# Kernel optimization log

Measured on AMD Instinct MI355X. Metric: run time of the kernel, lower is better.

The kernel has to match this reference:

```python
import jax, jax.numpy as jnp
import numpy as np

N = 50000
E = 800000
F0, F1, F2 = 256, 128, 64
EPS = 1e-5


def setup_inputs() -> dict:
    key = jax.random.key(0)
    ks = jax.random.split(key, 20)
    x = jax.random.normal(ks[0], (N, F0), dtype=jnp.float32)
    src = jax.random.randint(ks[1], (E,), 0, N)
    dst = jax.random.randint(ks[2], (E,), 0, N)
    edge_index = jnp.stack([src, dst]).astype(jnp.int64)

    def lin(k, fi, fo):
        s = 1.0 / np.sqrt(fi)
        k1, k2 = jax.random.split(k)
        W = jax.random.uniform(k1, (fi, fo), minval=-s, maxval=s, dtype=jnp.float32)
        b = jax.random.uniform(k2, (fo,), minval=-s, maxval=s, dtype=jnp.float32)
        return W, b

    We1, be1 = lin(ks[3], F0, F1)
    We2, be2 = lin(ks[4], F1, F2)
    Wd1, bd1 = lin(ks[5], F2, F1)
    Wd2, bd2 = lin(ks[6], F1, F0)
    return {
        'x': x, 'edge_index': edge_index,
        'We1': We1, 'be1': be1, 'g1': jnp.ones((F1,)), 'bb1': jnp.zeros((F1,)),
        'We2': We2, 'be2': be2, 'g2': jnp.ones((F2,)), 'bb2': jnp.zeros((F2,)),
        'Wd1': Wd1, 'bd1': bd1, 'g3': jnp.ones((F1,)), 'bb3': jnp.zeros((F1,)),
        'Wd2': Wd2, 'bd2': bd2, 'g4': jnp.ones((F0,)), 'bb4': jnp.zeros((F0,)),
    }


def _gcn(x, W, b, src, dst, dinv_src_dst, dinv_self):
    # PyG GCNConv: linear first, then sym-normalized propagation with self-loops
    h = x @ W + b                               # [N, Fout]
    msg = h[src] * dinv_src_dst[:, None]        # [E, Fout]
    out = jax.ops.segment_sum(msg, dst, num_segments=N)
    return out + h * dinv_self[:, None]         # self-loop term


def _bn(x, g, b):
    # BatchNorm1d training-mode: biased batch stats over node dim
    m = jnp.mean(x, axis=0)
    v = jnp.mean(jnp.square(x - m), axis=0)
    return g * (x - m) * jax.lax.rsqrt(v + EPS) + b


def reference(x, edge_index, We1, be1, g1, bb1, We2, be2, g2, bb2,
              Wd1, bd1, g3, bb3, Wd2, bd2, g4, bb4):
    src, dst = edge_index[0], edge_index[1]
    deg = jnp.zeros((N,), x.dtype).at[dst].add(1.0) + 1.0  # in-degree + self-loop
    dinv = jax.lax.rsqrt(deg)
    dsd = dinv[src] * dinv[dst]
    dself = dinv * dinv

    relu = jax.nn.relu
    # Encoder block 0 (outer i==0): relu(GCN), relu(BN)
    h = relu(_gcn(x, We1, be1, src, dst, dsd, dself))
    h = relu(_bn(h, g1, bb1))
    enc1 = h
    # Encoder block 1 (outer i==1 == len(inner)-1): relu(GCN), BN (no relu)
    h = relu(_gcn(h, We2, be2, src, dst, dsd, dself))
    h = _bn(h, g2, bb2)
    enc2 = h
    # Decoder block 0: relu(GCN), relu(BN)
    h = relu(_gcn(h, Wd1, bd1, src, dst, dsd, dself))
    h = relu(_bn(h, g3, bb3))
    # Decoder block 1 (i==1): relu(GCN), BN (no relu)
    h = relu(_gcn(h, Wd2, bd2, src, dst, dsd, dself))
    h = _bn(h, g4, bb4)
    # AE returns (reconstruction, encoded_embeddings)
    return h, enc1, enc2
```

## Files before the change

### kernel.cpp

```cpp
#include <hip/hip_runtime.h>

#define N_NODES 50000
#define F0 256
#define F1 128
#define F2 64
#define BN_EPS 1e-5f

typedef float f32x4 __attribute__((ext_vector_type(4)));
typedef __bf16 bf16x8 __attribute__((ext_vector_type(8)));
typedef unsigned short ushort8v __attribute__((ext_vector_type(8)));

__device__ __forceinline__ float bflo(unsigned v) { return __uint_as_float(v << 16); }
__device__ __forceinline__ float bfhi(unsigned v) { return __uint_as_float(v & 0xFFFF0000u); }
__device__ __forceinline__ unsigned short f2bf(float f) {
  unsigned u = __float_as_uint(f);
  u += 0x7FFFu + ((u >> 16) & 1u);
  return (unsigned short)(u >> 16);
}
__device__ __forceinline__ void split2(float a, unsigned short& hi, unsigned short& lo) {
  hi = f2bf(a);
  float hf = __uint_as_float((unsigned)hi << 16);
  lo = f2bf(a - hf);
}
__device__ __forceinline__ int rdl(int v, int l) { return __builtin_amdgcn_readlane(v, l); }
__device__ __forceinline__ float rdlf(float v, int l) {
  return __uint_as_float((unsigned)__builtin_amdgcn_readlane(__float_as_int(v), l));
}

__global__ void count_dst(const int* __restrict__ dst, int* __restrict__ counts, int E) {
  int e = blockIdx.x * blockDim.x + threadIdx.x;
  if (e < E) atomicAdd(&counts[dst[e]], 1);
}

__global__ void compute_dinv(const int* __restrict__ counts, float* __restrict__ dinv) {
  int i = blockIdx.x * blockDim.x + threadIdx.x;
  if (i < N_NODES) dinv[i] = rsqrtf((float)counts[i] + 1.0f);
}

__global__ __launch_bounds__(1024) void scan_offsets(const int* __restrict__ counts,
                                                     int* __restrict__ offs) {
  __shared__ int s_wsum[16];
  __shared__ int s_carry, s_total;
  int tid = threadIdx.x;
  int lane = tid & 63, wid = tid >> 6;
  if (tid == 0) s_carry = 0;
  __syncthreads();
  for (int base = 0; base < N_NODES; base += 1024) {
    int i = base + tid;
    int v = (i < N_NODES) ? counts[i] : 0;
    int incl = v;
#pragma unroll
    for (int d = 1; d < 64; d <<= 1) {
      int t = __shfl_up(incl, d);
      if (lane >= d) incl += t;
    }
    if (lane == 63) s_wsum[wid] = incl;
    __syncthreads();
    if (tid == 0) {
      int run = 0;
      for (int j = 0; j < 16; j++) { int t = s_wsum[j]; s_wsum[j] = run; run += t; }
      s_total = run;
    }
    __syncthreads();
    if (i < N_NODES) offs[i] = s_carry + s_wsum[wid] + incl - v;
    __syncthreads();
    if (tid == 0) s_carry += s_total;
    __syncthreads();
  }
  if (tid == 0) offs[N_NODES] = s_carry;
}

__global__ void fill_csr(const int* __restrict__ src, const int* __restrict__ dst,
                         const int* __restrict__ offs, int* __restrict__ cursor,
                         const float* __restrict__ dinv,
                         int* __restrict__ csr_src, float* __restrict__ csr_w, int E) {
  int e = blockIdx.x * blockDim.x + threadIdx.x;
  if (e < E) {
    int s = src[e], d = dst[e];
    int p = offs[d] + atomicAdd(&cursor[d], 1);
    csr_src[p] = s;
    csr_w[p] = dinv[s] * dinv[d];
  }
}

__global__ void compute_rowsum(const int* __restrict__ offs, const float* __restrict__ csr_w,
                               const float* __restrict__ dinv, float* __restrict__ rowsum) {
  int i = blockIdx.x * blockDim.x + threadIdx.x;
  if (i < N_NODES) {
    float s = dinv[i] * dinv[i];
    int e1 = offs[i + 1];
    for (int e = offs[i]; e < e1; e++) s += csr_w[e];
    rowsum[i] = s;
  }
}

__device__ __forceinline__ void wt_one(const float* W, unsigned short* Wh, unsigned short* Wl,
                                       int K, int N, int idx) {
  int k = idx / N, n = idx - k * N;
  unsigned short h, l;
  split2(W[idx], h, l);
  Wh[(size_t)n * K + k] = h;
  Wl[(size_t)n * K + k] = l;
}

__global__ void convert_weights(const float* __restrict__ We1, const float* __restrict__ We2,
                                const float* __restrict__ Wd1, const float* __restrict__ Wd2,
                                unsigned short* W1h, unsigned short* W1l,
                                unsigned short* W2h, unsigned short* W2l,
                                unsigned short* W3h, unsigned short* W3l,
                                unsigned short* W4h, unsigned short* W4l) {
  int idx = blockIdx.x * blockDim.x + threadIdx.x;
  if (idx < 32768) {
    wt_one(We1, W1h, W1l, 256, 128, idx);
  } else if (idx < 40960) {
    wt_one(We2, W2h, W2l, 128, 64, idx - 32768);
  } else if (idx < 49152) {
    wt_one(Wd1, W3h, W3l, 64, 128, idx - 40960);
  } else if (idx < 81920) {
    wt_one(Wd2, W4h, W4l, 128, 256, idx - 49152);
  }
}

template <int BN, bool STATS, bool AF32>
__global__ __launch_bounds__(256) void mfma_gemm_split(
    const unsigned short* __restrict__ Ahi, const unsigned short* __restrict__ Alo,
    const float* __restrict__ Af,
    const unsigned short* __restrict__ Whi, const unsigned short* __restrict__ Wlo,
    const float* __restrict__ bias, const float* __restrict__ rowsum,
    unsigned short* __restrict__ Cb, float* __restrict__ Cf,
    float* __restrict__ stat, int M, int K, int N) {
  constexpr int BM = 128;
  constexpr int MT = (BN == 128) ? 4 : 2;
  constexpr int NT = 4;
  __shared__ __align__(16) unsigned short AsH[4][BM][8];
  __shared__ __align__(16) unsigned short AsL[4][BM][8];
  __shared__ __align__(16) unsigned short BsH[4][BN][8];
  __shared__ __align__(16) unsigned short BsL[4][BN][8];
  const int tid = threadIdx.x;
  const int lane = tid & 63, wid = tid >> 6;
  const int quad = lane >> 4, ln = lane & 15;
  const int m0 = blockIdx.x * BM;
  const int n0 = blockIdx.y * BN;
  const int wm = (BN == 128) ? (wid & 1) * 64 : wid * 32;
  const int wn = (BN == 128) ? (wid >> 1) * 64 : 0;
  f32x4 acc[MT][NT] = {};

  const int arow = tid >> 2, aseg = tid & 3;
  for (int k0 = 0; k0 < K; k0 += 32) {
#pragma unroll
    for (int i = 0; i < 2; i++) {
      int row = arow + i * 64;
      int gm = m0 + row;
      if (AF32) {
        float4 u0 = make_float4(0.f, 0.f, 0.f, 0.f), u1 = u0;
        if (gm < M) {
          u0 = *(const float4*)(Af + (size_t)gm * K + k0 + aseg * 8);
          u1 = *(const float4*)(Af + (size_t)gm * K + k0 + aseg * 8 + 4);
        }
        ushort4 h0, l0, h1, l1;
        split2(u0.x, h0.x, l0.x); split2(u0.y, h0.y, l0.y);
        split2(u0.z, h0.z, l0.z); split2(u0.w, h0.w, l0.w);
        split2(u1.x, h1.x, l1.x); split2(u1.y, h1.y, l1.y);
        split2(u1.z, h1.z, l1.z); split2(u1.w, h1.w, l1.w);
        *(ushort4*)(&AsH[aseg][row][0]) = h0;
        *(ushort4*)(&AsH[aseg][row][4]) = h1;
        *(ushort4*)(&AsL[aseg][row][0]) = l0;
        *(ushort4*)(&AsL[aseg][row][4]) = l1;
      } else {
        ushort8v vh = {0, 0, 0, 0, 0, 0, 0, 0};
        ushort8v vl = {0, 0, 0, 0, 0, 0, 0, 0};
        if (gm < M) {
          vh = *(const ushort8v*)(Ahi + (size_t)gm * K + k0 + aseg * 8);
          vl = *(const ushort8v*)(Alo + (size_t)gm * K + k0 + aseg * 8);
        }
        *(ushort8v*)(&AsH[aseg][row][0]) = vh;
        *(ushort8v*)(&AsL[aseg][row][0]) = vl;
      }
    }
#pragma unroll
    for (int i = 0; i < BN / 64; i++) {
      int n = arow + i * 64;
      *(ushort8v*)(&BsH[aseg][n][0]) =
          *(const ushort8v*)(Whi + (size_t)(n0 + n) * K + k0 + aseg * 8);
      *(ushort8v*)(&BsL[aseg][n][0]) =
          *(const ushort8v*)(Wlo + (size_t)(n0 + n) * K + k0 + aseg * 8);
    }
    __syncthreads();
    bf16x8 ah[MT], al[MT], bh[NT], bl[NT];
#pragma unroll
    for (int mt = 0; mt < MT; mt++) {
      ah[mt] = *(const bf16x8*)(&AsH[quad][wm + mt * 16 + ln][0]);
      al[mt] = *(const bf16x8*)(&AsL[quad][wm + mt * 16 + ln][0]);
    }
#pragma unroll
    for (int nt = 0; nt < NT; nt++) {
      bh[nt] = *(const bf16x8*)(&BsH[quad][wn + nt * 16 + ln][0]);
      bl[nt] = *(const bf16x8*)(&BsL[quad][wn + nt * 16 + ln][0]);
    }
#pragma unroll
    for (int mt = 0; mt < MT; mt++)
#pragma unroll
      for (int nt = 0; nt < NT; nt++) {
        acc[mt][nt] = __builtin_amdgcn_mfma_f32_16x16x32_bf16(ah[mt], bl[nt], acc[mt][nt], 0, 0, 0);
        acc[mt][nt] = __builtin_amdgcn_mfma_f32_16x16x32_bf16(al[mt], bh[nt], acc[mt][nt], 0, 0, 0);
        acc[mt][nt] = __builtin_amdgcn_mfma_f32_16x16x32_bf16(ah[mt], bh[nt], acc[mt][nt], 0, 0, 0);
      }
    __syncthreads();
  }

  if (!STATS) {
#pragma unroll
    for (int nt = 0; nt < NT; nt++) {
      int gn = n0 + wn + nt * 16 + ln;
      float bv = bias[gn];
#pragma unroll
      for (int mt = 0; mt < MT; mt++) {
#pragma unroll
        for (int r = 0; r < 4; r++) {
          int gm = m0 + wm + mt * 16 + quad * 4 + r;
          if (gm < M) Cb[(size_t)gm * N + gn] = f2bf(acc[mt][nt][r] + bv);
        }
      }
    }
  } else {
    float rs[MT][4];
#pragma unroll
    for (int mt = 0; mt < MT; mt++)
#pragma unroll
      for (int r = 0; r < 4; r++) {
        int gm = m0 + wm + mt * 16 + quad * 4 + r;
        rs[mt][r] = (gm < M) ? rowsum[gm] : 0.f;
      }
#pragma unroll
    for (int nt = 0; nt < NT; nt++) {
      int gn = n0 + wn + nt * 16 + ln;
      float bv = bias[gn];
      float ls = 0.f, lq = 0.f;
#pragma unroll
      for (int mt = 0; mt < MT; mt++) {
#pragma unroll
        for (int r = 0; r < 4; r++) {
          int gm = m0 + wm + mt * 16 + quad * 4 + r;
          if (gm < M) {
            float v = fmaxf(fmaf(bv, rs[mt][r], acc[mt][nt][r]), 0.f);
            Cf[(size_t)gm * N + gn] = v;
            ls += v;
            lq = fmaf(v, v, lq);
          }
        }
      }
      ls += __shfl_xor(ls, 16); ls += __shfl_xor(ls, 32);
      lq += __shfl_xor(lq, 16); lq += __shfl_xor(lq, 32);
      if (quad == 0) {
        atomicAdd(&stat[gn], ls);
        atomicAdd(&stat[256 + gn], lq);
      }
    }
  }
}

template <bool RELU_STATS, bool OUT_SPLIT>
__global__ __launch_bounds__(256) void agg128_rl(
    const unsigned short* __restrict__ hb, const int* __restrict__ offs,
    const int* __restrict__ csr_src, const float* __restrict__ csr_w,
    const float* __restrict__ dinv, float* __restrict__ outf,
    unsigned short* __restrict__ outhi, unsigned short* __restrict__ outlo,
    float* __restrict__ stat) {
  const int tid = threadIdx.x;
  const int lane = tid & 63;
  const int widx = tid >> 6;
  const int nwaves = gridDim.x * 4;
  float ls0 = 0.f, ls1 = 0.f, lq0 = 0.f, lq1 = 0.f;

  for (int node = blockIdx.x * 4 + widx; node < N_NODES; node += nwaves) {
    const int e0 = __builtin_amdgcn_readfirstlane(offs[node]);
    const int e1 = __builtin_amdgcn_readfirstlane(offs[node + 1]);
    float a0 = 0.f, a1 = 0.f;
    for (int e = e0; e < e1; e += 64) {
      const int cnt = min(64, e1 - e);
      int idx = 0;
      float wt = 0.f;
      if (lane < cnt) {
        idx = csr_src[e + lane];
        wt = csr_w[e + lane];
      }
      const int nb = (cnt + 7) & ~7;
      for (int j = 0; j < nb; j += 8) {
#pragma unroll
        for (int u = 0; u < 8; u++) {
          int s = rdl(idx, j + u);
          float w = rdlf(wt, j + u);
          unsigned v = *(const unsigned*)(hb + (size_t)s * 128 + lane * 2);
          a0 = fmaf(bflo(v), w, a0);
          a1 = fmaf(bfhi(v), w, a1);
        }
      }
    }
    float di = dinv[node];
    float ds = di * di;
    unsigned vs = *(const unsigned*)(hb + (size_t)node * 128 + lane * 2);
    a0 = fmaf(bflo(vs), ds, a0);
    a1 = fmaf(bfhi(vs), ds, a1);
    if (RELU_STATS) {
      a0 = fmaxf(a0, 0.f);
      a1 = fmaxf(a1, 0.f);
      ls0 += a0; ls1 += a1;
      lq0 = fmaf(a0, a0, lq0);
      lq1 = fmaf(a1, a1, lq1);
    }
    if (OUT_SPLIT) {
      unsigned short h0, l0, h1, l1;
      split2(a0, h0, l0);
      split2(a1, h1, l1);
      *(unsigned*)(outhi + (size_t)node * 128 + lane * 2) = (unsigned)h0 | ((unsigned)h1 << 16);
      *(unsigned*)(outlo + (size_t)node * 128 + lane * 2) = (unsigned)l0 | ((unsigned)l1 << 16);
    } else {
      *(float2*)(outf + (size_t)node * 128 + lane * 2) = make_float2(a0, a1);
    }
  }

  if (RELU_STATS) {
    __shared__ float red[4][128];
    red[widx][lane * 2 + 0] = ls0;
    red[widx][lane * 2 + 1] = ls1;
    __syncthreads();
    if (tid < 128) {
      atomicAdd(&stat[tid], red[0][tid] + red[1][tid] + red[2][tid] + red[3][tid]);
    }
    __syncthreads();
    red[widx][lane * 2 + 0] = lq0;
    red[widx][lane * 2 + 1] = lq1;
    __syncthreads();
    if (tid < 128) {
      atomicAdd(&stat[256 + tid], red[0][tid] + red[1][tid] + red[2][tid] + red[3][tid]);
    }
  }
}

template <bool RELU_STATS, bool OUT_SPLIT>
__global__ __launch_bounds__(256) void agg64_rl(
    const unsigned short* __restrict__ hb, const int* __restrict__ offs,
    const int* __restrict__ csr_src, const float* __restrict__ csr_w,
    const float* __restrict__ dinv, float* __restrict__ outf,
    unsigned short* __restrict__ outhi, unsigned short* __restrict__ outlo,
    float* __restrict__ stat) {
  const int tid = threadIdx.x;
  const int lane = tid & 63;
  const int widx = tid >> 6;
  const int half = lane >> 5;
  const int hl = lane & 31;
  const int nwaves = gridDim.x * 4;
  float ls0 = 0.f, ls1 = 0.f, lq0 = 0.f, lq1 = 0.f;

  for (int node = blockIdx.x * 4 + widx; node < N_NODES; node += nwaves) {
    const int e0 = __builtin_amdgcn_readfirstlane(offs[node]);
    const int e1 = __builtin_amdgcn_readfirstlane(offs[node + 1]);
    float a0 = 0.f, a1 = 0.f;
    for (int e = e0; e < e1; e += 64) {
      const int cnt = min(64, e1 - e);
      int idx = 0;
      float wt = 0.f;
      if (lane < cnt) {
        idx = csr_src[e + lane];
        wt = csr_w[e + lane];
      }
      const int nb = (cnt + 15) & ~15;
      for (int j = 0; j < nb; j += 16) {
#pragma unroll
        for (int u = 0; u < 8; u++) {
          int sa = rdl(idx, j + 2 * u);
          int sb = rdl(idx, j + 2 * u + 1);
          float wa = rdlf(wt, j + 2 * u);
          float wb = rdlf(wt, j + 2 * u + 1);
          const unsigned short* pa = hb + (size_t)sa * 64;
          const unsigned short* pb = hb + (size_t)sb * 64;
          const unsigned short* p = half ? pb : pa;
          float w = half ? wb : wa;
          unsigned v = *(const unsigned*)(p + hl * 2);
          a0 = fmaf(bflo(v), w, a0);
          a1 = fmaf(bfhi(v), w, a1);
        }
      }
    }
    a0 += __shfl_xor(a0, 32);
    a1 += __shfl_xor(a1, 32);
    float di = dinv[node];
    float ds = di * di;
    unsigned vs = *(const unsigned*)(hb + (size_t)node * 64 + hl * 2);
    a0 = fmaf(bflo(vs), ds, a0);
    a1 = fmaf(bfhi(vs), ds, a1);
    if (RELU_STATS) {
      a0 = fmaxf(a0, 0.f);
      a1 = fmaxf(a1, 0.f);
      if (half == 0) {
        ls0 += a0; ls1 += a1;
        lq0 = fmaf(a0, a0, lq0);
        lq1 = fmaf(a1, a1, lq1);
      }
    }
    if (half == 0) {
      if (OUT_SPLIT) {
        unsigned short h0, l0, h1, l1;
        split2(a0, h0, l0);
        split2(a1, h1, l1);
        *(unsigned*)(outhi + (size_t)node * 64 + hl * 2) = (unsigned)h0 | ((unsigned)h1 << 16);
        *(unsigned*)(outlo + (size_t)node * 64 + hl * 2) = (unsigned)l0 | ((unsigned)l1 << 16);
      } else {
        *(float2*)(outf + (size_t)node * 64 + hl * 2) = make_float2(a0, a1);
      }
    }
  }

  if (RELU_STATS) {
    __shared__ float red[4][64];
    if (half == 0) {
      red[widx][hl * 2 + 0] = ls0;
      red[widx][hl * 2 + 1] = ls1;
    }
    __syncthreads();
    if (tid < 64) {
      atomicAdd(&stat[tid], red[0][tid] + red[1][tid] + red[2][tid] + red[3][tid]);
    }
    __syncthreads();
    if (half == 0) {
      red[widx][hl * 2 + 0] = lq0;
      red[widx][hl * 2 + 1] = lq1;
    }
    __syncthreads();
    if (tid < 64) {
      atomicAdd(&stat[256 + tid], red[0][tid] + red[1][tid] + red[2][tid] + red[3][tid]);
    }
  }
}

template <int F, bool RELU, bool WF32, bool WB16, bool WSPLIT>
__global__ __launch_bounds__(256) void bn_apply_f(const float* __restrict__ a,
                                                  const float* __restrict__ stat,
                                                  const float* __restrict__ g,
                                                  const float* __restrict__ bb,
                                                  float* __restrict__ outf,
                                                  unsigned short* __restrict__ outb,
                                                  unsigned short* __restrict__ outhi,
                                                  unsigned short* __restrict__ outlo) {
  __shared__ float s_scale[F], s_shift[F];
  const int tid = threadIdx.x;
  if (tid < F) {
    const float invN = 1.0f / (float)N_NODES;
    float mean = stat[tid] * invN;
    float var = fmaxf(stat[256 + tid] * invN - mean * mean, 0.f);
    float inv = rsqrtf(var + BN_EPS);
    float sc = g[tid] * inv;
    s_scale[tid] = sc;
    s_shift[tid] = bb[tid] - mean * sc;
  }
  __syncthreads();
  constexpr int C4 = F / 4;
  const int total = N_NODES * C4;
  for (int idx = blockIdx.x * blockDim.x + tid; idx < total; idx += gridDim.x * blockDim.x) {
    int c4 = idx % C4;
    float4 v = ((const float4*)a)[idx];
    float4 s = *(float4*)&s_scale[c4 * 4];
    float4 sh = *(float4*)&s_shift[c4 * 4];
    float4 o;
    o.x = fmaf(v.x, s.x, sh.x);
    o.y = fmaf(v.y, s.y, sh.y);
    o.z = fmaf(v.z, s.z, sh.z);
    o.w = fmaf(v.w, s.w, sh.w);
    if (RELU) {
      o.x = fmaxf(o.x, 0.f);
      o.y = fmaxf(o.y, 0.f);
      o.z = fmaxf(o.z, 0.f);
      o.w = fmaxf(o.w, 0.f);
    }
    if (WF32) ((float4*)outf)[idx] = o;
    if (WB16) {
      ushort4 b;
      b.x = f2bf(o.x); b.y = f2bf(o.y); b.z = f2bf(o.z); b.w = f2bf(o.w);
      ((ushort4*)outb)[idx] = b;
    }
    if (WSPLIT) {
      ushort4 h, l;
      split2(o.x, h.x, l.x);
      split2(o.y, h.y, l.y);
      split2(o.z, h.z, l.z);
      split2(o.w, h.w, l.w);
      ((ushort4*)outhi)[idx] = h;
      ((ushort4*)outlo)[idx] = l;
    }
  }
}

extern "C" void kernel_launch(void* const* d_in, const int* in_sizes, int n_in,
                              void* d_out, int out_size, void* d_ws, size_t ws_size,
                              hipStream_t stream) {
  const float* x = (const float*)d_in[0];
  const int* ei = (const int*)d_in[1];
  const int E = in_sizes[1] / 2;
  const int* src = ei;
  const int* dst = ei + E;
  const float* We1 = (const float*)d_in[2];  const float* be1 = (const float*)d_in[3];
  const float* g1  = (const float*)d_in[4];  const float* bb1 = (const float*)d_in[5];
  const float* We2 = (const float*)d_in[6];  const float* be2 = (const float*)d_in[7];
  const float* g2  = (const float*)d_in[8];  const float* bb2 = (const float*)d_in[9];
  const float* Wd1 = (const float*)d_in[10]; const float* bd1 = (const float*)d_in[11];
  const float* g3  = (const float*)d_in[12]; const float* bb3 = (const float*)d_in[13];
  const float* Wd2 = (const float*)d_in[14]; const float* bd2 = (const float*)d_in[15];
  const float* g4  = (const float*)d_in[16]; const float* bb4 = (const float*)d_in[17];

  float* out = (float*)d_out;
  char* ws = (char*)d_ws;
  unsigned short* A0b  = (unsigned short*)(ws + 0);
  unsigned short* A1b  = (unsigned short*)(ws + 12800000);
  unsigned short* C2b  = (unsigned short*)(ws + 32000000);
  unsigned short* G3hi = (unsigned short*)(ws + 0);
  unsigned short* G3lo = (unsigned short*)(ws + 6400000);
  unsigned short* D3b  = (unsigned short*)(ws + 12800000);
  unsigned short* G4hi = (unsigned short*)(ws + 0);
  unsigned short* G4lo = (unsigned short*)(ws + 25600000);
  unsigned short* Wb   = (unsigned short*)(ws + 48000000);
  unsigned short* W1h = Wb;            unsigned short* W1l = W1h + 32768;
  unsigned short* W2h = W1l + 32768;   unsigned short* W2l = W2h + 8192;
  unsigned short* W3h = W2l + 8192;    unsigned short* W3l = W3h + 8192;
  unsigned short* W4h = W3l + 8192;    unsigned short* W4l = W4h + 32768;
  float* B0f  = (float*)(ws + 51200000);
  int*   csrS   = (int*)(ws + 102400000);
  float* csrW   = (float*)(ws + 105600000);
  float* stat4  = (float*)(ws + 108800000);
  int*   counts = (int*)(ws + 108810000);
  int*   cursor = (int*)(ws + 109010000);
  int*   offs   = (int*)(ws + 109210000);
  float* dinv   = (float*)(ws + 109410064);
  if (ws_size < 109604160) return;
  float* rowsum = (float*)cursor;

  float* enc1 = out + (size_t)N_NODES * F0;
  float* enc2 = enc1 + (size_t)N_NODES * F1;

  const int EB = (E + 255) / 256;
  const int AGG_GRID = 2048;
  const int MB = (N_NODES + 127) / 128;

  convert_weights<<<320, 256, 0, stream>>>(We1, We2, Wd1, Wd2, W1h, W1l, W2h, W2l,
                                           W3h, W3l, W4h, W4l);
  hipMemsetAsync(counts, 0, 2 * N_NODES * sizeof(int) + 20000, stream);
  hipMemsetAsync(stat4, 0, 4 * 512 * sizeof(float), stream);
  count_dst<<<EB, 256, 0, stream>>>(dst, counts, E);
  compute_dinv<<<(N_NODES + 255) / 256, 256, 0, stream>>>(counts, dinv);
  scan_offsets<<<1, 1024, 0, stream>>>(counts, offs);
  fill_csr<<<EB, 256, 0, stream>>>(src, dst, offs, cursor, dinv, csrS, csrW, E);
  compute_rowsum<<<(N_NODES + 255) / 256, 256, 0, stream>>>(offs, csrW, dinv, rowsum);

  mfma_gemm_split<128, false, true><<<dim3(MB, 1), 256, 0, stream>>>(
      nullptr, nullptr, x, W1h, W1l, be1, nullptr, A0b, nullptr, nullptr, N_NODES, F0, F1);
  agg128_rl<true, false><<<AGG_GRID, 256, 0, stream>>>(
      A0b, offs, csrS, csrW, dinv, B0f, nullptr, nullptr, stat4);
  bn_apply_f<F1, true, true, false, false><<<2048, 256, 0, stream>>>(
      B0f, stat4, g1, bb1, enc1, nullptr, nullptr, nullptr);

  mfma_gemm_split<64, false, true><<<dim3(MB, 1), 256, 0, stream>>>(
      nullptr, nullptr, enc1, W2h, W2l, be2, nullptr, A1b, nullptr, nullptr, N_NODES, F1, F2);
  agg64_rl<true, false><<<AGG_GRID, 256, 0, stream>>>(
      A1b, offs, csrS, csrW, dinv, B0f, nullptr, nullptr, stat4 + 512);
  bn_apply_f<F2, false, true, true, false><<<2048, 256, 0, stream>>>(
      B0f, stat4 + 512, g2, bb2, enc2, C2b, nullptr, nullptr);

  agg64_rl<false, true><<<AGG_GRID, 256, 0, stream>>>(
      C2b, offs, csrS, csrW, dinv, nullptr, G3hi, G3lo, nullptr);
  mfma_gemm_split<128, true, false><<<dim3(MB, 1), 256, 0, stream>>>(
      G3hi, G3lo, nullptr, W3h, W3l, bd1, rowsum, nullptr, B0f, stat4 + 1024, N_NODES, F2, F1);
  bn_apply_f<F1, true, false, true, false><<<2048, 256, 0, stream>>>(
      B0f, stat4 + 1024, g3, bb3, nullptr, D3b, nullptr, nullptr);

  agg128_rl<false, true><<<AGG_GRID, 256, 0, stream>>>(
      D3b, offs, csrS, csrW, dinv, nullptr, G4hi, G4lo, nullptr);
  mfma_gemm_split<128, true, false><<<dim3(MB, 2), 256, 0, stream>>>(
      G4hi, G4lo, nullptr, W4h, W4l, bd2, rowsum, nullptr, B0f, stat4 + 1536, N_NODES, F1, F0);
  bn_apply_f<F0, false, true, false, false><<<2048, 256, 0, stream>>>(
      B0f, stat4 + 1536, g4, bb4, out, nullptr, nullptr, nullptr);
}
```

Baseline: 651.6 us.

## Parallelize CSR offset scan and widen per-lane gathers in aggregation kernels

Result: no change. 642.6 us (-1.4%).

```diff
diff --git a/kernel.cpp b/kernel.cpp
--- a/kernel.cpp
+++ b/kernel.cpp
@@ -32,42 +32,78 @@
   if (e < E) atomicAdd(&counts[dst[e]], 1);
 }
 
-__global__ void compute_dinv(const int* __restrict__ counts, float* __restrict__ dinv) {
-  int i = blockIdx.x * blockDim.x + threadIdx.x;
-  if (i < N_NODES) dinv[i] = rsqrtf((float)counts[i] + 1.0f);
-}
-
-__global__ __launch_bounds__(1024) void scan_offsets(const int* __restrict__ counts,
-                                                     int* __restrict__ offs) {
-  __shared__ int s_wsum[16];
-  __shared__ int s_carry, s_total;
-  int tid = threadIdx.x;
-  int lane = tid & 63, wid = tid >> 6;
-  if (tid == 0) s_carry = 0;
+__global__ __launch_bounds__(256) void scan_blocks(const int* __restrict__ counts,
+                                                   int* __restrict__ offs,
+                                                   int* __restrict__ bsum,
+                                                   float* __restrict__ dinv) {
+  __shared__ int s_w[4];
+  const int tid = threadIdx.x, lane = tid & 63, wid = tid >> 6;
+  const int base = blockIdx.x * 1024 + tid * 4;
+  int v0 = 0, v1 = 0, v2 = 0, v3 = 0;
+  if (base + 3 < N_NODES) {
+    int4 v = *(const int4*)(counts + base);
+    v0 = v.x; v1 = v.y; v2 = v.z; v3 = v.w;
+  } else if (base < N_NODES) {
+    v0 = counts[base];
+    if (base + 1 < N_NODES) v1 = counts[base + 1];
+    if (base + 2 < N_NODES) v2 = counts[base + 2];
+  }
+  if (base < N_NODES) {
+    dinv[base] = rsqrtf((float)v0 + 1.0f);
+    if (base + 1 < N_NODES) dinv[base + 1] = rsqrtf((float)v1 + 1.0f);
+    if (base + 2 < N_NODES) dinv[base + 2] = rsqrtf((float)v2 + 1.0f);
+    if (base + 3 < N_NODES) dinv[base + 3] = rsqrtf((float)v3 + 1.0f);
+  }
+  int t = v0 + v1 + v2 + v3;
+  int incl = t;
+#pragma unroll
+  for (int d = 1; d < 64; d <<= 1) {
+    int x = __shfl_up(incl, d);
+    if (lane >= d) incl += x;
+  }
+  if (lane == 63) s_w[wid] = incl;
   __syncthreads();
-  for (int base = 0; base < N_NODES; base += 1024) {
-    int i = base + tid;
-    int v = (i < N_NODES) ? counts[i] : 0;
-    int incl = v;
-#pragma unroll
-    for (int d = 1; d < 64; d <<= 1) {
-      int t = __shfl_up(incl, d);
-      if (lane >= d) incl += t;
-    }
-    if (lane == 63) s_wsum[wid] = incl;
-    __syncthreads();
-    if (tid == 0) {
-      int run = 0;
-      for (int j = 0; j < 16; j++) { int t = s_wsum[j]; s_wsum[j] = run; run += t; }
-      s_total = run;
-    }
-    __syncthreads();
-    if (i < N_NODES) offs[i] = s_carry + s_wsum[wid] + incl - v;
-    __syncthreads();
-    if (tid == 0) s_carry += s_total;
-    __syncthreads();
-  }
-  if (tid == 0) offs[N_NODES] = s_carry;
+  int woff = 0;
+#pragma unroll
+  for (int j = 0; j < 4; j++)
+    if (j < wid) woff += s_w[j];
+  int p = woff + incl - t;
+  if (base < N_NODES) offs[base] = p;
+  p += v0;
+  if (base + 1 < N_NODES) offs[base + 1] = p;
+  p += v1;
+  if (base + 2 < N_NODES) offs[base + 2] = p;
+  p += v2;
+  if (base + 3 < N_NODES) offs[base + 3] = p;
+  if (tid == 255) bsum[blockIdx.x] = woff + incl;
+}
+
+__global__ void scan_tops(int* __restrict__ bsum, int* __restrict__ offs, int nblk) {
+  int lane = threadIdx.x;
+  int v = (lane < nblk) ? bsum[lane] : 0;
+  int incl = v;
+#pragma unroll
+  for (int d = 1; d < 64; d <<= 1) {
+    int x = __shfl_up(incl, d);
+    if (lane >= d) incl += x;
+  }
+  if (lane < nblk) bsum[lane] = incl - v;
+  if (lane == 63) offs[N_NODES] = incl;
+}
+
+__global__ __launch_bounds__(256) void scan_add(int* __restrict__ offs,
+                                                const int* __restrict__ bsum) {
+  const int add = bsum[blockIdx.x];
+  const int base = blockIdx.x * 1024 + threadIdx.x * 4;
+  if (base + 3 < N_NODES) {
+    int4 v = *(const int4*)(offs + base);
+    v.x += add; v.y += add; v.z += add; v.w += add;
+    *(int4*)(offs + base) = v;
+  } else if (base < N_NODES) {
+    offs[base] += add;
+    if (base + 1 < N_NODES) offs[base + 1] += add;
+    if (base + 2 < N_NODES) offs[base + 2] += add;
+  }
 }
 
 __global__ void fill_csr(const int* __restrict__ src, const int* __restrict__ dst,
@@ -269,13 +305,16 @@
   const int tid = threadIdx.x;
   const int lane = tid & 63;
   const int widx = tid >> 6;
+  const int half = lane >> 5;
+  const int hl = lane & 31;
   const int nwaves = gridDim.x * 4;
-  float ls0 = 0.f, ls1 = 0.f, lq0 = 0.f, lq1 = 0.f;
+  float ls0 = 0.f, ls1 = 0.f, ls2 = 0.f, ls3 = 0.f;
+  float lq0 = 0.f, lq1 = 0.f, lq2 = 0.f, lq3 = 0.f;
 
   for (int node = blockIdx.x * 4 + widx; node < N_NODES; node += nwaves) {
     const int e0 = __builtin_amdgcn_readfirstlane(offs[node]);
     const int e1 = __builtin_amdgcn_readfirstlane(offs[node + 1]);
-    float a0 = 0.f, a1 = 0.f;
+    float a0 = 0.f, a1 = 0.f, a2 = 0.f, a3 = 0.f;
     for (int e = e0; e < e1; e += 64) {
       const int cnt = min(64, e1 - e);
       int idx = 0;
@@ -284,52 +323,85 @@
         idx = csr_src[e + lane];
         wt = csr_w[e + lane];
       }
-      const int nb = (cnt + 7) & ~7;
-      for (int j = 0; j < nb; j += 8) {
+      const int nb = (cnt + 15) & ~15;
+      for (int j = 0; j < nb; j += 16) {
 #pragma unroll
         for (int u = 0; u < 8; u++) {
-          int s = rdl(idx, j + u);
-          float w = rdlf(wt, j + u);
-          unsigned v = *(const unsigned*)(hb + (size_t)s * 128 + lane * 2);
-          a0 = fmaf(bflo(v), w, a0);
-          a1 = fmaf(bfhi(v), w, a1);
+          int sa = rdl(idx, j + 2 * u);
+          int sb = rdl(idx, j + 2 * u + 1);
+          float wa = rdlf(wt, j + 2 * u);
+          float wb = rdlf(wt, j + 2 * u + 1);
+          int s = half ? sb : sa;
+          float w = half ? wb : wa;
+          uint2 v = *(const uint2*)(hb + (size_t)s * 128 + hl * 4);
+          a0 = fmaf(bflo(v.x), w, a0);
+          a1 = fmaf(bfhi(v.x), w, a1);
+          a2 = fmaf(bflo(v.y), w, a2);
+          a3 = fmaf(bfhi(v.y), w, a3);
         }
       }
     }
+    a0 += __shfl_xor(a0, 32);
+    a1 += __shfl_xor(a1, 32);
+    a2 += __shfl_xor(a2, 32);
+    a3 += __shfl_xor(a3, 32);
     float di = dinv[node];
     float ds = di * di;
-    unsigned vs = *(const unsigned*)(hb + (size_t)node * 128 + lane * 2);
-    a0 = fmaf(bflo(vs), ds, a0);
-    a1 = fmaf(bfhi(vs), ds, a1);
+    uint2 vs = *(const uint2*)(hb + (size_t)node * 128 + hl * 4);
+    a0 = fmaf(bflo(vs.x), ds, a0);
+    a1 = fmaf(bfhi(vs.x), ds, a1);
+    a2 = fmaf(bflo(vs.y), ds, a2);
+    a3 = fmaf(bfhi(vs.y), ds, a3);
     if (RELU_STATS) {
       a0 = fmaxf(a0, 0.f);
       a1 = fmaxf(a1, 0.f);
-      ls0 += a0; ls1 += a1;
-      lq0 = fmaf(a0, a0, lq0);
-      lq1 = fmaf(a1, a1, lq1);
-    }
-    if (OUT_SPLIT) {
-      unsigned short h0, l0, h1, l1;
-      split2(a0, h0, l0);
-      split2(a1, h1, l1);
-      *(unsigned*)(outhi + (size_t)node * 128 + lane * 2) = (unsigned)h0 | ((unsigned)h1 << 16);
-      *(unsigned*)(outlo + (size_t)node * 128 + lane * 2) = (unsigned)l0 | ((unsigned)l1 << 16);
-    } else {
-      *(float2*)(outf + (size_t)node * 128 + lane * 2) = make_float2(a0, a1);
+      a2 = fmaxf(a2, 0.f);
+      a3 = fmaxf(a3, 0.f);
+      if (half == 0) {
+        ls0 += a0; ls1 += a1; ls2 += a2; ls3 += a3;
+        lq0 = fmaf(a0, a0, lq0);
+        lq1 = fmaf(a1, a1, lq1);
+        lq2 = fmaf(a2, a2, lq2);
+        lq3 = fmaf(a3, a3, lq3);
+      }
+    }
+    if (half == 0) {
+      if (OUT_SPLIT) {
+        unsigned short h0, l0, h1, l1, h2, l2, h3, l3;
+        split2(a0, h0, l0);
+        split2(a1, h1, l1);
+        split2(a2, h2, l2);
+        split2(a3, h3, l3);
+        ushort4 hv, lv;
+        hv.x = h0; hv.y = h1; hv.z = h2; hv.w = h3;
+        lv.x = l0; lv.y = l1; lv.z = l2; lv.w = l3;
+        *(ushort4*)(outhi + (size_t)node * 128 + hl * 4) = hv;
+        *(ushort4*)(outlo + (size_t)node * 128 + hl * 4) = lv;
+      } else {
+        *(float4*)(outf + (size_t)node * 128 + hl * 4) = make_float4(a0, a1, a2, a3);
+      }
     }
   }
 
   if (RELU_STATS) {
     __shared__ float red[4][128];
-    red[widx][lane * 2 + 0] = ls0;
-    red[widx][lane * 2 + 1] = ls1;
+    if (half == 0) {
+      red[widx][hl * 4 + 0] = ls0;
+      red[widx][hl * 4 + 1] = ls1;
+      red[widx][hl * 4 + 2] = ls2;
+      red[widx][hl * 4 + 3] = ls3;
+    }
     __syncthreads();
     if (tid < 128) {
       atomicAdd(&stat[tid], red[0][tid] + red[1][tid] + red[2][tid] + red[3][tid]);
     }
     __syncthreads();
-    red[widx][lane * 2 + 0] = lq0;
-    red[widx][lane * 2 + 1] = lq1;
+    if (half == 0) {
+      red[widx][hl * 4 + 0] = lq0;
+      red[widx][hl * 4 + 1] = lq1;
+      red[widx][hl * 4 + 2] = lq2;
+      red[widx][hl * 4 + 3] = lq3;
+    }
     __syncthreads();
     if (tid < 128) {
       atomicAdd(&stat[256 + tid], red[0][tid] + red[1][tid] + red[2][tid] + red[3][tid]);
@@ -347,15 +419,15 @@
   const int tid = threadIdx.x;
   const int lane = tid & 63;
   const int widx = tid >> 6;
-  const int half = lane >> 5;
-  const int hl = lane & 31;
+  const int ql = lane & 15;
   const int nwaves = gridDim.x * 4;
-  float ls0 = 0.f, ls1 = 0.f, lq0 = 0.f, lq1 = 0.f;
+  float ls0 = 0.f, ls1 = 0.f, ls2 = 0.f, ls3 = 0.f;
+  float lq0 = 0.f, lq1 = 0.f, lq2 = 0.f, lq3 = 0.f;
 
   for (int node = blockIdx.x * 4 + widx; node < N_NODES; node += nwaves) {
     const int e0 = __builtin_amdgcn_readfirstlane(offs[node]);
     const int e1 = __builtin_amdgcn_readfirstlane(offs[node + 1]);
-    float a0 = 0.f, a1 = 0.f;
+    float a0 = 0.f, a1 = 0.f, a2 = 0.f, a3 = 0.f;
     for (int e = e0; e < e1; e += 64) {
       const int cnt = min(64, e1 - e);
       int idx = 0;
@@ -364,67 +436,92 @@
         idx = csr_src[e + lane];
         wt = csr_w[e + lane];
       }
-      const int nb = (cnt + 15) & ~15;
-      for (int j = 0; j < nb; j += 16) {
+      const int nb = (cnt + 31) & ~31;
+      for (int j = 0; j < nb; j += 32) {
 #pragma unroll
         for (int u = 0; u < 8; u++) {
-          int sa = rdl(idx, j + 2 * u);
-          int sb = rdl(idx, j + 2 * u + 1);
-          float wa = rdlf(wt, j + 2 * u);
-          float wb = rdlf(wt, j + 2 * u + 1);
-          const unsigned short* pa = hb + (size_t)sa * 64;
-          const unsigned short* pb = hb + (size_t)sb * 64;
-          const unsigned short* p = half ? pb : pa;
-          float w = half ? wb : wa;
-          unsigned v = *(const unsigned*)(p + hl * 2);
-          a0 = fmaf(bflo(v), w, a0);
-          a1 = fmaf(bfhi(v), w, a1);
+          int s0 = rdl(idx, j + 4 * u + 0);
+          int s1 = rdl(idx, j + 4 * u + 1);
+          int s2 = rdl(idx, j + 4 * u + 2);
+          int s3 = rdl(idx, j + 4 * u + 3);
+          float w0 = rdlf(wt, j + 4 * u + 0);
+          float w1 = rdlf(wt, j + 4 * u + 1);
+          float w2 = rdlf(wt, j + 4 * u + 2);
+          float w3 = rdlf(wt, j + 4 * u + 3);
+          int sx = (lane & 16) ? s1 : s0;
+          int sy = (lane & 16) ? s3 : s2;
+          int s = (lane & 32) ? sy : sx;
+          float wx = (lane & 16) ? w1 : w0;
+          float wy = (lane & 16) ? w3 : w2;
+          float w = (lane & 32) ? wy : wx;
+          uint2 v = *(const uint2*)(hb + (size_t)s * 64 + ql * 4);
+          a0 = fmaf(bflo(v.x), w, a0);
+          a1 = fmaf(bfhi(v.x), w, a1);
+          a2 = fmaf(bflo(v.y), w, a2);
+          a3 = fmaf(bfhi(v.y), w, a3);
         }
       }
     }
-    a0 += __shfl_xor(a0, 32);
-    a1 += __shfl_xor(a1, 32);
+    a0 += __shfl_xor(a0, 16); a0 += __shfl_xor(a0, 32);
+    a1 += __shfl_xor(a1, 16); a1 += __shfl_xor(a1, 32);
+    a2 += __shfl_xor(a2, 16); a2 += __shfl_xor(a2, 32);
+    a3 += __shfl_xor(a3, 16); a3 += __shfl_xor(a3, 32);
     float di = dinv[node];
     float ds = di * di;
-    unsigned vs = *(const unsigned*)(hb + (size_t)node * 64 + hl * 2);
-    a0 = fmaf(bflo(vs), ds, a0);
-    a1 = fmaf(bfhi(vs), ds, a1);
+    uint2 vs = *(const uint2*)(hb + (size_t)node * 64 + ql * 4);
+    a0 = fmaf(bflo(vs.x), ds, a0);
+    a1 = fmaf(bfhi(vs.x), ds, a1);
+    a2 = fmaf(bflo(vs.y), ds, a2);
+    a3 = fmaf(bfhi(vs.y), ds, a3);
     if (RELU_STATS) {
       a0 = fmaxf(a0, 0.f);
       a1 = fmaxf(a1, 0.f);
-      if (half == 0) {
-        ls0 += a0; ls1 += a1;
+      a2 = fmaxf(a2, 0.f);
+      a3 = fmaxf(a3, 0.f);
+      if (lane < 16) {
+        ls0 += a0; ls1 += a1; ls2 += a2; ls3 += a3;
         lq0 = fmaf(a0, a0, lq0);
         lq1 = fmaf(a1, a1, lq1);
-      }
-    }
-    if (half == 0) {
+        lq2 = fmaf(a2, a2, lq2);
+        lq3 = fmaf(a3, a3, lq3);
+      }
+    }
+    if (lane < 16) {
       if (OUT_SPLIT) {
-        unsigned short h0, l0, h1, l1;
+        unsigned short h0, l0, h1, l1, h2, l2, h3, l3;
         split2(a0, h0, l0);
         split2(a1, h1, l1);
-        *(unsigned*)(outhi + (size_t)node * 64 + hl * 2) = (unsigned)h0 | ((unsigned)h1 << 16);
-        *(unsigned*)(outlo + (size_t)node * 64 + hl * 2) = (unsigned)l0 | ((unsigned)l1 << 16);
+        split2(a2, h2, l2);
+        split2(a3, h3, l3);
+        ushort4 hv, lv;
+        hv.x = h0; hv.y = h1; hv.z = h2; hv.w = h3;
+        lv.x = l0; lv.y = l1; lv.z = l2; lv.w = l3;
+        *(ushort4*)(outhi + (size_t)node * 64 + ql * 4) = hv;
+        *(ushort4*)(outlo + (size_t)node * 64 + ql * 4) = lv;
       } else {
-        *(float2*)(outf + (size_t)node * 64 + hl * 2) = make_float2(a0, a1);
+        *(float4*)(outf + (size_t)node * 64 + ql * 4) = make_float4(a0, a1, a2, a3);
       }
     }
   }
 
   if (RELU_STATS) {
     __shared__ float red[4][64];
-    if (half == 0) {
-      red[widx][hl * 2 + 0] = ls0;
-      red[widx][hl * 2 + 1] = ls1;
+    if (lane < 16) {
+      red[widx][ql * 4 + 0] = ls0;
+      red[widx][ql * 4 + 1] = ls1;
+      red[widx][ql * 4 + 2] = ls2;
+      red[widx][ql * 4 + 3] = ls3;
     }
     __syncthreads();
     if (tid < 64) {
       atomicAdd(&stat[tid], red[0][tid] + red[1][tid] + red[2][tid] + red[3][tid]);
     }
     __syncthreads();
-    if (half == 0) {
-      red[widx][hl * 2 + 0] = lq0;
-      red[widx][hl * 2 + 1] = lq1;
+    if (lane < 16) {
+      red[widx][ql * 4 + 0] = lq0;
+      red[widx][ql * 4 + 1] = lq1;
+      red[widx][ql * 4 + 2] = lq2;
+      red[widx][ql * 4 + 3] = lq3;
     }
     __syncthreads();
     if (tid < 64) {
@@ -526,6 +623,7 @@
   int*   csrS   = (int*)(ws + 102400000);
   float* csrW   = (float*)(ws + 105600000);
   float* stat4  = (float*)(ws + 108800000);
+  int*   bsum   = (int*)(ws + 108808192);
   int*   counts = (int*)(ws + 108810000);
   int*   cursor = (int*)(ws + 109010000);
   int*   offs   = (int*)(ws + 109210000);
@@ -539,14 +637,16 @@
   const int EB = (E + 255) / 256;
   const int AGG_GRID = 2048;
   const int MB = (N_NODES + 127) / 128;
+  const int SCAN_B = (N_NODES + 1023) / 1024;
 
   convert_weights<<<320, 256, 0, stream>>>(We1, We2, Wd1, Wd2, W1h, W1l, W2h, W2l,
                                            W3h, W3l, W4h, W4l);
   hipMemsetAsync(counts, 0, 2 * N_NODES * sizeof(int) + 20000, stream);
   hipMemsetAsync(stat4, 0, 4 * 512 * sizeof(float), stream);
   count_dst<<<EB, 256, 0, stream>>>(dst, counts, E);
-  compute_dinv<<<(N_NODES + 255) / 256, 256, 0, stream>>>(counts, dinv);
-  scan_offsets<<<1, 1024, 0, stream>>>(counts, offs);
+  scan_blocks<<<SCAN_B, 256, 0, stream>>>(counts, offs, bsum, dinv);
+  scan_tops<<<1, 64, 0, stream>>>(bsum, offs, SCAN_B);
+  scan_add<<<SCAN_B, 256, 0, stream>>>(offs, bsum);
   fill_csr<<<EB, 256, 0, stream>>>(src, dst, offs, cursor, dinv, csrS, csrW, E);
   compute_rowsum<<<(N_NODES + 255) / 256, 256, 0, stream>>>(offs, csrW, dinv, rowsum);
 
```

## Parallelize CSR offset scan across blocks and fold rowsum into fill_csr

Applied to the files above, without the earlier changes.

Result: no change. 639.4 us (-1.9%).

```diff
diff --git a/kernel.cpp b/kernel.cpp
--- a/kernel.cpp
+++ b/kernel.cpp
@@ -32,65 +32,101 @@
   if (e < E) atomicAdd(&counts[dst[e]], 1);
 }
 
-__global__ void compute_dinv(const int* __restrict__ counts, float* __restrict__ dinv) {
-  int i = blockIdx.x * blockDim.x + threadIdx.x;
-  if (i < N_NODES) dinv[i] = rsqrtf((float)counts[i] + 1.0f);
-}
-
-__global__ __launch_bounds__(1024) void scan_offsets(const int* __restrict__ counts,
-                                                     int* __restrict__ offs) {
-  __shared__ int s_wsum[16];
-  __shared__ int s_carry, s_total;
-  int tid = threadIdx.x;
-  int lane = tid & 63, wid = tid >> 6;
-  if (tid == 0) s_carry = 0;
+__global__ __launch_bounds__(256) void scan_blocks(const int* __restrict__ counts,
+                                                   int* __restrict__ offs,
+                                                   int* __restrict__ bsum,
+                                                   float* __restrict__ dinv) {
+  __shared__ int s_w[4];
+  const int tid = threadIdx.x, lane = tid & 63, wid = tid >> 6;
+  const int base = blockIdx.x * 1024 + tid * 4;
+  int v0 = 0, v1 = 0, v2 = 0, v3 = 0;
+  if (base + 3 < N_NODES) {
+    int4 v = *(const int4*)(counts + base);
+    v0 = v.x; v1 = v.y; v2 = v.z; v3 = v.w;
+  } else if (base < N_NODES) {
+    v0 = counts[base];
+    if (base + 1 < N_NODES) v1 = counts[base + 1];
+    if (base + 2 < N_NODES) v2 = counts[base + 2];
+  }
+  if (base < N_NODES) {
+    dinv[base] = rsqrtf((float)v0 + 1.0f);
+    if (base + 1 < N_NODES) dinv[base + 1] = rsqrtf((float)v1 + 1.0f);
+    if (base + 2 < N_NODES) dinv[base + 2] = rsqrtf((float)v2 + 1.0f);
+    if (base + 3 < N_NODES) dinv[base + 3] = rsqrtf((float)v3 + 1.0f);
+  }
+  int t = v0 + v1 + v2 + v3;
+  int incl = t;
+#pragma unroll
+  for (int d = 1; d < 64; d <<= 1) {
+    int x = __shfl_up(incl, d);
+    if (lane >= d) incl += x;
+  }
+  if (lane == 63) s_w[wid] = incl;
   __syncthreads();
-  for (int base = 0; base < N_NODES; base += 1024) {
-    int i = base + tid;
-    int v = (i < N_NODES) ? counts[i] : 0;
-    int incl = v;
-#pragma unroll
-    for (int d = 1; d < 64; d <<= 1) {
-      int t = __shfl_up(incl, d);
-      if (lane >= d) incl += t;
-    }
-    if (lane == 63) s_wsum[wid] = incl;
-    __syncthreads();
-    if (tid == 0) {
-      int run = 0;
-      for (int j = 0; j < 16; j++) { int t = s_wsum[j]; s_wsum[j] = run; run += t; }
-      s_total = run;
-    }
-    __syncthreads();
-    if (i < N_NODES) offs[i] = s_carry + s_wsum[wid] + incl - v;
-    __syncthreads();
-    if (tid == 0) s_carry += s_total;
-    __syncthreads();
-  }
-  if (tid == 0) offs[N_NODES] = s_carry;
+  int woff = 0;
+#pragma unroll
+  for (int j = 0; j < 4; j++)
+    if (j < wid) woff += s_w[j];
+  int p = woff + incl - t;
+  if (base < N_NODES) offs[base] = p;
+  p += v0;
+  if (base + 1 < N_NODES) offs[base + 1] = p;
+  p += v1;
+  if (base + 2 < N_NODES) offs[base + 2] = p;
+  p += v2;
+  if (base + 3 < N_NODES) offs[base + 3] = p;
+  if (tid == 255) bsum[blockIdx.x] = woff + incl;
+}
+
+__global__ void scan_tops(int* __restrict__ bsum, int* __restrict__ offs, int nblk) {
+  int lane = threadIdx.x;
+  int v = (lane < nblk) ? bsum[lane] : 0;
+  int incl = v;
+#pragma unroll
+  for (int d = 1; d < 64; d <<= 1) {
+    int x = __shfl_up(incl, d);
+    if (lane >= d) incl += x;
+  }
+  if (lane < nblk) bsum[lane] = incl - v;
+  if (lane == 63) offs[N_NODES] = incl;
+}
+
+__global__ __launch_bounds__(256) void scan_add(int* __restrict__ offs,
+                                                const int* __restrict__ bsum,
+                                                const float* __restrict__ dinv,
+                                                float* __restrict__ rowsum) {
+  const int add = bsum[blockIdx.x];
+  const int base = blockIdx.x * 1024 + threadIdx.x * 4;
+  if (base + 3 < N_NODES) {
+    int4 v = *(const int4*)(offs + base);
+    v.x += add; v.y += add; v.z += add; v.w += add;
+    *(int4*)(offs + base) = v;
+    float4 d = *(const float4*)(dinv + base);
+    float4 r;
+    r.x = d.x * d.x; r.y = d.y * d.y; r.z = d.z * d.z; r.w = d.w * d.w;
+    *(float4*)(rowsum + base) = r;
+  } else if (base < N_NODES) {
+    for (int k = 0; k < 4 && base + k < N_NODES; k++) {
+      offs[base + k] += add;
+      float d = dinv[base + k];
+      rowsum[base + k] = d * d;
+    }
+  }
 }
 
 __global__ void fill_csr(const int* __restrict__ src, const int* __restrict__ dst,
                          const int* __restrict__ offs, int* __restrict__ cursor,
                          const float* __restrict__ dinv,
-                         int* __restrict__ csr_src, float* __restrict__ csr_w, int E) {
+                         int* __restrict__ csr_src, float* __restrict__ csr_w,
+                         float* __restrict__ rowsum, int E) {
   int e = blockIdx.x * blockDim.x + threadIdx.x;
   if (e < E) {
     int s = src[e], d = dst[e];
     int p = offs[d] + atomicAdd(&cursor[d], 1);
+    float w = dinv[s] * dinv[d];
     csr_src[p] = s;
-    csr_w[p] = dinv[s] * dinv[d];
-  }
-}
-
-__global__ void compute_rowsum(const int* __restrict__ offs, const float* __restrict__ csr_w,
-                               const float* __restrict__ dinv, float* __restrict__ rowsum) {
-  int i = blockIdx.x * blockDim.x + threadIdx.x;
-  if (i < N_NODES) {
-    float s = dinv[i] * dinv[i];
-    int e1 = offs[i + 1];
-    for (int e = offs[i]; e < e1; e++) s += csr_w[e];
-    rowsum[i] = s;
+    csr_w[p] = w;
+    atomicAdd(&rowsum[d], w);
   }
 }
 
@@ -526,12 +562,13 @@
   int*   csrS   = (int*)(ws + 102400000);
   float* csrW   = (float*)(ws + 105600000);
   float* stat4  = (float*)(ws + 108800000);
+  int*   bsum   = (int*)(ws + 108808192);
   int*   counts = (int*)(ws + 108810000);
   int*   cursor = (int*)(ws + 109010000);
   int*   offs   = (int*)(ws + 109210000);
   float* dinv   = (float*)(ws + 109410064);
   if (ws_size < 109604160) return;
-  float* rowsum = (float*)cursor;
+  float* rowsum = (float*)counts;
 
   float* enc1 = out + (size_t)N_NODES * F0;
   float* enc2 = enc1 + (size_t)N_NODES * F1;
@@ -539,16 +576,17 @@
   const int EB = (E + 255) / 256;
   const int AGG_GRID = 2048;
   const int MB = (N_NODES + 127) / 128;
+  const int SCAN_B = (N_NODES + 1023) / 1024;
 
   convert_weights<<<320, 256, 0, stream>>>(We1, We2, Wd1, Wd2, W1h, W1l, W2h, W2l,
                                            W3h, W3l, W4h, W4l);
-  hipMemsetAsync(counts, 0, 2 * N_NODES * sizeof(int) + 20000, stream);
+  hipMemsetAsync(counts, 0, 400000, stream);
   hipMemsetAsync(stat4, 0, 4 * 512 * sizeof(float), stream);
   count_dst<<<EB, 256, 0, stream>>>(dst, counts, E);
-  compute_dinv<<<(N_NODES + 255) / 256, 256, 0, stream>>>(counts, dinv);
-  scan_offsets<<<1, 1024, 0, stream>>>(counts, offs);
-  fill_csr<<<EB, 256, 0, stream>>>(src, dst, offs, cursor, dinv, csrS, csrW, E);
-  compute_rowsum<<<(N_NODES + 255) / 256, 256, 0, stream>>>(offs, csrW, dinv, rowsum);
+  scan_blocks<<<SCAN_B, 256, 0, stream>>>(counts, offs, bsum, dinv);
+  scan_tops<<<1, 64, 0, stream>>>(bsum, offs, SCAN_B);
+  scan_add<<<SCAN_B, 256, 0, stream>>>(offs, bsum, dinv, rowsum);
+  fill_csr<<<EB, 256, 0, stream>>>(src, dst, offs, cursor, dinv, csrS, csrW, rowsum, E);
 
   mfma_gemm_split<128, false, true><<<dim3(MB, 1), 256, 0, stream>>>(
       nullptr, nullptr, x, W1h, W1l, be1, nullptr, A0b, nullptr, nullptr, N_NODES, F0, F1);
```
